# Performance work log

Measured on AMD Instinct MI355X. Metric: run time of the kernel, lower is better.

Reference implementation:

```python
import jax, jax.numpy as jnp
import numpy as np

B, Q, S, T, HID, NH = 4, 64, 64, 128, 768, 12
HD = HID // NH  # 64
SCALE = 1.0 / (HD ** 0.5)
EPS = 1e-12


def setup_inputs() -> dict:
    key = jax.random.key(0)
    ks = jax.random.split(key, 12)
    std = 0.02
    return {
        "ini_q": jax.random.normal(ks[0], (B, Q, HID), jnp.float32),
        "ini_k": jax.random.normal(ks[1], (B, S, T, HID), jnp.float32),
        "mask": jax.random.randint(ks[2], (B, S, T), 0, 2).astype(jnp.float32),
        "Wq": jax.random.normal(ks[3], (HID, HID), jnp.float32) * std,
        "bq": jnp.zeros((HID,), jnp.float32),
        "Wk": jax.random.normal(ks[4], (HID, HID), jnp.float32) * std,
        "bk": jnp.zeros((HID,), jnp.float32),
        "Wv": jax.random.normal(ks[5], (HID, HID), jnp.float32) * std,
        "bv": jnp.zeros((HID,), jnp.float32),
        "Wo": jax.random.normal(ks[6], (HID, HID), jnp.float32) * std,
        "bo": jnp.zeros((HID,), jnp.float32),
        "gamma": jnp.ones((HID,), jnp.float32),
        "beta": jnp.zeros((HID,), jnp.float32),
    }


def reference(ini_q, ini_k, mask, Wq, bq, Wk, bk, Wv, bv, Wo, bo, gamma, beta):
    b, q_num, _ = ini_q.shape
    _, s_num, t_num, _ = ini_k.shape
    # projections (torch Linear: x @ W.T + b; here W stored pre-transposed)
    q = (ini_q @ Wq + bq).reshape(b, q_num, NH, HD)          # [b,q,h,d]
    k = (ini_k @ Wk + bk).reshape(b, s_num, t_num, NH, HD)   # [b,s,t,h,d]
    v = (ini_k @ Wv + bv).reshape(b, s_num, t_num, NH, HD)
    # non-aligned path: scores [b,h,q,s,t]
    scores = jnp.einsum('bqhd,bsthd->bhqst', q, k) * SCALE
    scores = scores + mask[:, None, None, :, :] * (-10000.0)
    alpha = jax.nn.softmax(scores, axis=-1)
    res = jnp.einsum('bhqst,bsthd->bqshd', alpha, v)          # [b,q,s,h,d]
    res = res.reshape(b, q_num, s_num, NH * HD)
    res = res @ Wo + bo                                        # [b,q,s,hid]
    # LayerNorm over last dim
    mu = jnp.mean(res, axis=-1, keepdims=True)
    var = jnp.var(res, axis=-1, keepdims=True)
    return (res - mu) / jnp.sqrt(var + EPS) * gamma + beta
```

## Files before the change

### kernel.cpp

```cpp
#include <hip/hip_runtime.h>
#include <cstdint>
#include <cstddef>
#include <type_traits>

#define HID 768
#define NB 4
#define NQ 64
#define NS 64
#define NT 128
#define NHEAD 12
#define HD 64

typedef __attribute__((ext_vector_type(8))) short bf16x8;
typedef __attribute__((ext_vector_type(4))) float f32x4;

__device__ __forceinline__ unsigned short f2bf(float f) {
    union { float f; uint32_t u; } c; c.f = f;
    uint32_t x = c.u;
    uint32_t r = (x + 0x7FFFu + ((x >> 16) & 1u)) >> 16;
    return (unsigned short)r;
}

__device__ __forceinline__ f32x4 mfma16(bf16x8 a, bf16x8 b, f32x4 c) {
    return __builtin_amdgcn_mfma_f32_16x16x32_bf16(a, b, c, 0, 0, 0);
}

__device__ __forceinline__ void gload_lds16(const void* g, void* l) {
    __builtin_amdgcn_global_load_lds(
        (const __attribute__((address_space(1))) unsigned int*)g,
        (__attribute__((address_space(3))) unsigned int*)l, 16, 0, 0);
}

__global__ __launch_bounds__(256) void cast4_f32_bf16(const float* __restrict__ in,
                                                      unsigned short* __restrict__ out, int n4) {
    int i = blockIdx.x * 256 + threadIdx.x;
    if (i < n4) {
        float4 v = ((const float4*)in)[i];
        ushort4 o;
        o.x = f2bf(v.x); o.y = f2bf(v.y); o.z = f2bf(v.z); o.w = f2bf(v.w);
        ((ushort4*)out)[i] = o;
    }
}

__global__ __launch_bounds__(256) void transpose_cast_768(const float* __restrict__ W,
                                                          unsigned short* __restrict__ Wt) {
    __shared__ float t[32][33];
    int bx = blockIdx.x % 24, by = blockIdx.x / 24;
    int n0 = bx * 32, k0 = by * 32;
    int tx = threadIdx.x & 31, ty = threadIdx.x >> 5;
#pragma unroll
    for (int i = 0; i < 4; ++i)
        t[ty + i * 8][tx] = W[(size_t)(k0 + ty + i * 8) * 768 + n0 + tx];
    __syncthreads();
#pragma unroll
    for (int i = 0; i < 4; ++i)
        Wt[(size_t)(n0 + ty + i * 8) * 768 + k0 + tx] = f2bf(t[tx][ty + i * 8]);
}

template <typename CT>
__global__ __launch_bounds__(256) void gemm_bt_768(const unsigned short* __restrict__ A,
                                                   const unsigned short* __restrict__ Bt,
                                                   const float* __restrict__ bias,
                                                   CT* __restrict__ C, int M) {
    constexpr int K = 768, N = 768;
    __shared__ __align__(16) unsigned short As[128 * 32];
    __shared__ __align__(16) unsigned short Bs[128 * 32];

    int tid = threadIdx.x;
    int w = tid >> 6, l = tid & 63;
    int li = l & 15, g = l >> 4;
    int wm = w >> 1, wn = w & 1;
    int nb = blockIdx.x % (N / 128);
    int mb = blockIdx.x / (N / 128);

    const unsigned short* Ab = A + (size_t)mb * 128 * K;
    const unsigned short* Bb = Bt + (size_t)nb * 128 * K;

    int ch0 = w * 128 + l, ch1 = w * 128 + 64 + l;
    int r0 = ch0 >> 2, c0 = ch0 & 3;
    int r1 = ch1 >> 2, c1 = ch1 & 3;
    char* lA0 = (char*)As + w * 2048;
    char* lA1 = (char*)As + w * 2048 + 1024;
    char* lB0 = (char*)Bs + w * 2048;
    char* lB1 = (char*)Bs + w * 2048 + 1024;

    f32x4 acc[4][4];
#pragma unroll
    for (int mi = 0; mi < 4; ++mi)
#pragma unroll
        for (int ni = 0; ni < 4; ++ni) acc[mi][ni] = (f32x4){0.f, 0.f, 0.f, 0.f};

    for (int kt = 0; kt < K / 32; ++kt) {
        int k0 = kt * 32;
        __syncthreads();
        gload_lds16(Ab + (size_t)r0 * K + k0 + c0 * 8, lA0);
        gload_lds16(Ab + (size_t)r1 * K + k0 + c1 * 8, lA1);
        gload_lds16(Bb + (size_t)r0 * K + k0 + c0 * 8, lB0);
        gload_lds16(Bb + (size_t)r1 * K + k0 + c1 * 8, lB1);
        __syncthreads();

        bf16x8 af[4], bb[4];
#pragma unroll
        for (int mi = 0; mi < 4; ++mi)
            af[mi] = *(const bf16x8*)&As[(wm * 64 + mi * 16 + li) * 32 + g * 8];
#pragma unroll
        for (int ni = 0; ni < 4; ++ni)
            bb[ni] = *(const bf16x8*)&Bs[(wn * 64 + ni * 16 + li) * 32 + g * 8];
#pragma unroll
        for (int mi = 0; mi < 4; ++mi)
#pragma unroll
            for (int ni = 0; ni < 4; ++ni)
                acc[mi][ni] = mfma16(af[mi], bb[ni], acc[mi][ni]);
    }

    int rowb = mb * 128 + wm * 64;
    int colb = nb * 128 + wn * 64;
#pragma unroll
    for (int ni = 0; ni < 4; ++ni) {
        float bv = bias[colb + ni * 16 + li];
        int col = colb + ni * 16 + li;
#pragma unroll
        for (int mi = 0; mi < 4; ++mi) {
#pragma unroll
            for (int r = 0; r < 4; ++r) {
                int row = rowb + mi * 16 + g * 4 + r;
                float v = acc[mi][ni][r] + bv;
                if constexpr (std::is_same_v<CT, unsigned short>)
                    C[(size_t)row * N + col] = f2bf(v);
                else
                    C[(size_t)row * N + col] = v;
            }
        }
    }
}

__global__ __launch_bounds__(256) void attn_bsh(const unsigned short* __restrict__ Qp,
                                                const unsigned short* __restrict__ Kb,
                                                const unsigned short* __restrict__ Vb,
                                                const float* __restrict__ mask,
                                                unsigned short* __restrict__ res) {
    __shared__ __align__(16) unsigned short Kl[128 * 72];
    __shared__ __align__(16) unsigned short VT[64 * 136];
    __shared__ __align__(16) unsigned short QA[64 * 136];

    int bid = blockIdx.x;
    int h = bid % NHEAD;
    int bs = bid / NHEAD;
    int s = bs % NS;
    int b = bs / NS;

    int tid = threadIdx.x, w = tid >> 6, l = tid & 63;
    int li = l & 15, g = l >> 4;

    const unsigned short* Qg = Qp + (size_t)(b * NQ) * HID + h * HD;
#pragma unroll
    for (int it = 0; it < 2; ++it) {
        int idx = it * 256 + tid;
        int q = idx >> 3, c = idx & 7;
        *(uint4*)&QA[q * 72 + c * 8] = *(const uint4*)&Qg[(size_t)q * HID + c * 8];
    }
    const unsigned short* Kg = Kb + ((size_t)(b * NS + s) * NT) * HID + h * HD;
#pragma unroll
    for (int it = 0; it < 4; ++it) {
        int idx = it * 256 + tid;
        int t = idx >> 3, c = idx & 7;
        *(uint4*)&Kl[t * 72 + c * 8] = *(const uint4*)&Kg[(size_t)t * HID + c * 8];
    }
    const unsigned short* Vg = Vb + ((size_t)(b * NS + s) * NT) * HID + h * HD;
#pragma unroll
    for (int it = 0; it < 4; ++it) {
        int idx = it * 256 + tid;
        int t = idx >> 3, c = idx & 7;
        uint4 raw = *(const uint4*)&Vg[(size_t)t * HID + c * 8];
        const unsigned short* e = (const unsigned short*)&raw;
#pragma unroll
        for (int j = 0; j < 8; ++j) VT[(c * 8 + j) * 136 + t] = e[j];
    }
    __syncthreads();

    bf16x8 aq0 = *(const bf16x8*)&QA[(w * 16 + li) * 72 + g * 8];
    bf16x8 aq1 = *(const bf16x8*)&QA[(w * 16 + li) * 72 + 32 + g * 8];
    f32x4 sc[8];
#pragma unroll
    for (int tc = 0; tc < 8; ++tc) {
        sc[tc] = (f32x4){0.f, 0.f, 0.f, 0.f};
        bf16x8 b0 = *(const bf16x8*)&Kl[(tc * 16 + li) * 72 + g * 8];
        sc[tc] = mfma16(aq0, b0, sc[tc]);
        bf16x8 b1 = *(const bf16x8*)&Kl[(tc * 16 + li) * 72 + 32 + g * 8];
        sc[tc] = mfma16(aq1, b1, sc[tc]);
    }

    const float* mrow = mask + (size_t)(b * NS + s) * NT;
    float mv[8];
#pragma unroll
    for (int tc = 0; tc < 8; ++tc) mv[tc] = mrow[tc * 16 + li] * -10000.0f;

    float p[8][4];
    float rmax[4] = {-3.0e38f, -3.0e38f, -3.0e38f, -3.0e38f};
#pragma unroll
    for (int tc = 0; tc < 8; ++tc)
#pragma unroll
        for (int r = 0; r < 4; ++r) {
            float v = sc[tc][r] * 0.125f + mv[tc];
            p[tc][r] = v;
            rmax[r] = fmaxf(rmax[r], v);
        }
#pragma unroll
    for (int r = 0; r < 4; ++r)
#pragma unroll
        for (int m = 1; m < 16; m <<= 1)
            rmax[r] = fmaxf(rmax[r], __shfl_xor(rmax[r], m, 64));

    float rsum[4] = {0.f, 0.f, 0.f, 0.f};
#pragma unroll
    for (int tc = 0; tc < 8; ++tc)
#pragma unroll
        for (int r = 0; r < 4; ++r) {
            float e = __expf(p[tc][r] - rmax[r]);
            p[tc][r] = e;
            rsum[r] += e;
        }
#pragma unroll
    for (int r = 0; r < 4; ++r)
#pragma unroll
        for (int m = 1; m < 16; m <<= 1)
            rsum[r] += __shfl_xor(rsum[r], m, 64);
    float rinv[4];
#pragma unroll
    for (int r = 0; r < 4; ++r) rinv[r] = 1.0f / rsum[r];

    __syncthreads();
#pragma unroll
    for (int tc = 0; tc < 8; ++tc)
#pragma unroll
        for (int r = 0; r < 4; ++r)
            QA[(w * 16 + g * 4 + r) * 136 + tc * 16 + li] = f2bf(p[tc][r] * rinv[r]);
    __syncthreads();

    bf16x8 pa[4];
#pragma unroll
    for (int ks = 0; ks < 4; ++ks)
        pa[ks] = *(const bf16x8*)&QA[(w * 16 + li) * 136 + ks * 32 + g * 8];
    f32x4 o[4];
#pragma unroll
    for (int dc = 0; dc < 4; ++dc) {
        o[dc] = (f32x4){0.f, 0.f, 0.f, 0.f};
#pragma unroll
        for (int ks = 0; ks < 4; ++ks) {
            bf16x8 bv = *(const bf16x8*)&VT[(dc * 16 + li) * 136 + ks * 32 + g * 8];
            o[dc] = mfma16(pa[ks], bv, o[dc]);
        }
    }

#pragma unroll
    for (int dc = 0; dc < 4; ++dc) {
#pragma unroll
        for (int r = 0; r < 4; ++r) {
            int q = w * 16 + g * 4 + r;
            int d = dc * 16 + li;
            res[((size_t)(b * NQ + q) * NS + s) * HID + h * HD + d] = f2bf(o[dc][r]);
        }
    }
}

__global__ __launch_bounds__(256) void ln_768(const float* __restrict__ X,
                                              const float* __restrict__ gamma,
                                              const float* __restrict__ beta,
                                              float* __restrict__ out) {
    int w = threadIdx.x >> 6, l = threadIdx.x & 63;
    size_t row = (size_t)blockIdx.x * 4 + w;
    const float4* xr = (const float4*)(X + row * 768);
    float4 v[3];
    float s = 0.f, sq = 0.f;
#pragma unroll
    for (int j = 0; j < 3; ++j) {
        v[j] = xr[l + j * 64];
        s += v[j].x + v[j].y + v[j].z + v[j].w;
        sq += v[j].x * v[j].x + v[j].y * v[j].y + v[j].z * v[j].z + v[j].w * v[j].w;
    }
#pragma unroll
    for (int m = 32; m >= 1; m >>= 1) {
        s += __shfl_xor(s, m, 64);
        sq += __shfl_xor(sq, m, 64);
    }
    float mu = s * (1.0f / 768.0f);
    float var = sq * (1.0f / 768.0f) - mu * mu;
    float rstd = rsqrtf(fmaxf(var, 0.0f) + 1e-12f);
    const float4* g4 = (const float4*)gamma;
    const float4* b4 = (const float4*)beta;
    float4* o4 = (float4*)(out + row * 768);
#pragma unroll
    for (int j = 0; j < 3; ++j) {
        float4 gg = g4[l + j * 64], bb = b4[l + j * 64];
        float4 r;
        r.x = (v[j].x - mu) * rstd * gg.x + bb.x;
        r.y = (v[j].y - mu) * rstd * gg.y + bb.y;
        r.z = (v[j].z - mu) * rstd * gg.z + bb.z;
        r.w = (v[j].w - mu) * rstd * gg.w + bb.w;
        o4[l + j * 64] = r;
    }
}

extern "C" void kernel_launch(void* const* d_in, const int* in_sizes, int n_in,
                              void* d_out, int out_size, void* d_ws, size_t ws_size,
                              hipStream_t stream) {
    const float* ini_q = (const float*)d_in[0];
    const float* ini_k = (const float*)d_in[1];
    const float* mask  = (const float*)d_in[2];
    const float* Wq = (const float*)d_in[3];
    const float* bq = (const float*)d_in[4];
    const float* Wk = (const float*)d_in[5];
    const float* bk = (const float*)d_in[6];
    const float* Wv = (const float*)d_in[7];
    const float* bv = (const float*)d_in[8];
    const float* Wo = (const float*)d_in[9];
    const float* bo = (const float*)d_in[10];
    const float* gamma = (const float*)d_in[11];
    const float* beta  = (const float*)d_in[12];
    float* out = (float*)d_out;

    constexpr size_t SZ_X = (size_t)32768 * 768 * 2;
    constexpr size_t SZ_R = (size_t)16384 * 768 * 2;
    constexpr size_t SZ_Q = (size_t)256 * 768 * 2;
    constexpr size_t SZ_W = (size_t)768 * 768 * 2;

    char* base = (char*)d_ws;
    unsigned short* X   = (unsigned short*)(base);
    unsigned short* Kb  = (unsigned short*)(base + SZ_X);
    unsigned short* Vb  = (unsigned short*)(base + 2 * SZ_X);
    unsigned short* res = (unsigned short*)(base + 3 * SZ_X);
    unsigned short* Xq  = (unsigned short*)(base + 3 * SZ_X + SZ_R);
    unsigned short* Qp  = (unsigned short*)(base + 3 * SZ_X + SZ_R + SZ_Q);
    unsigned short* WqT = (unsigned short*)(base + 3 * SZ_X + SZ_R + 2 * SZ_Q);
    unsigned short* WkT = (unsigned short*)((char*)WqT + SZ_W);
    unsigned short* WvT = (unsigned short*)((char*)WqT + 2 * SZ_W);
    unsigned short* WoT = (unsigned short*)((char*)WqT + 3 * SZ_W);
    float* res2 = (float*)(base);

    cast4_f32_bf16<<<24576, 256, 0, stream>>>(ini_k, X, 6291456);
    cast4_f32_bf16<<<192, 256, 0, stream>>>(ini_q, Xq, 49152);
    transpose_cast_768<<<576, 256, 0, stream>>>(Wq, WqT);
    transpose_cast_768<<<576, 256, 0, stream>>>(Wk, WkT);
    transpose_cast_768<<<576, 256, 0, stream>>>(Wv, WvT);
    transpose_cast_768<<<576, 256, 0, stream>>>(Wo, WoT);

    gemm_bt_768<unsigned short><<<dim3(2 * 6), 256, 0, stream>>>(Xq, WqT, bq, Qp, 256);
    gemm_bt_768<unsigned short><<<dim3(256 * 6), 256, 0, stream>>>(X, WkT, bk, Kb, 32768);
    gemm_bt_768<unsigned short><<<dim3(256 * 6), 256, 0, stream>>>(X, WvT, bv, Vb, 32768);

    attn_bsh<<<dim3(NB * NS * NHEAD), 256, 0, stream>>>(Qp, Kb, Vb, mask, res);

    gemm_bt_768<float><<<dim3(128 * 6), 256, 0, stream>>>(res, WoT, bo, res2, 16384);
    ln_768<<<dim3(4096), 256, 0, stream>>>(res2, gamma, beta, out);
}
```

Before: 421.2 us.

## Double-buffer GEMM LDS tiles, fuse K/V projections, and swizzle block order

The bf16 GEMM kernel now double-buffers its LDS tiles, so the global-to-LDS load for the next k-step is issued before the MFMA work on the current one, which hides load latency and removes one barrier per iteration. The K and V projections are merged into one GEMM over a concatenated 1536-wide transposed weight, and the epilogue routes each column to the K or V output, so the input X is streamed once instead of twice. Block IDs are remapped in groups of 8 when the grid size allows, presumably for better cache or XCD locality. LDS use per block doubles, which may reduce occupancy.

```diff
diff --git a/kernel.cpp b/kernel.cpp
--- a/kernel.cpp
+++ b/kernel.cpp
@@ -57,32 +57,50 @@
         Wt[(size_t)(n0 + ty + i * 8) * 768 + k0 + tx] = f2bf(t[tx][ty + i * 8]);
 }
 
-template <typename CT>
-__global__ __launch_bounds__(256) void gemm_bt_768(const unsigned short* __restrict__ A,
+template <typename CT, bool SPLIT>
+__global__ __launch_bounds__(256) void gemm_bt_2ph(const unsigned short* __restrict__ A,
                                                    const unsigned short* __restrict__ Bt,
-                                                   const float* __restrict__ bias,
-                                                   CT* __restrict__ C, int M) {
-    constexpr int K = 768, N = 768;
-    __shared__ __align__(16) unsigned short As[128 * 32];
-    __shared__ __align__(16) unsigned short Bs[128 * 32];
+                                                   const float* __restrict__ bias0,
+                                                   const float* __restrict__ bias1,
+                                                   CT* __restrict__ C0,
+                                                   CT* __restrict__ C1,
+                                                   int ncb) {
+    constexpr int K = 768;
+    constexpr int NKT = K / 32;
+    __shared__ __align__(16) unsigned short As[2][128 * 32];
+    __shared__ __align__(16) unsigned short Bs[2][128 * 32];
 
     int tid = threadIdx.x;
     int w = tid >> 6, l = tid & 63;
     int li = l & 15, g = l >> 4;
     int wm = w >> 1, wn = w & 1;
-    int nb = blockIdx.x % (N / 128);
-    int mb = blockIdx.x / (N / 128);
+
+    int nwg = gridDim.x, bid = blockIdx.x;
+    if ((nwg & 7) == 0) {
+        int cpx = nwg >> 3;
+        bid = (bid & 7) * cpx + (bid >> 3);
+    }
+    int nb = bid % ncb, mb = bid / ncb;
 
     const unsigned short* Ab = A + (size_t)mb * 128 * K;
     const unsigned short* Bb = Bt + (size_t)nb * 128 * K;
 
-    int ch0 = w * 128 + l, ch1 = w * 128 + 64 + l;
+    int ch0 = w * 128 + l, ch1 = ch0 + 64;
     int r0 = ch0 >> 2, c0 = ch0 & 3;
     int r1 = ch1 >> 2, c1 = ch1 & 3;
-    char* lA0 = (char*)As + w * 2048;
-    char* lA1 = (char*)As + w * 2048 + 1024;
-    char* lB0 = (char*)Bs + w * 2048;
-    char* lB1 = (char*)Bs + w * 2048 + 1024;
+
+#define STAGE(bufi, kt)                                                              \
+    do {                                                                             \
+        int k0_ = (kt) * 32;                                                         \
+        gload_lds16(Ab + (size_t)r0 * K + k0_ + c0 * 8,                              \
+                    (char*)(&As[bufi][0]) + w * 2048);                               \
+        gload_lds16(Ab + (size_t)r1 * K + k0_ + c1 * 8,                              \
+                    (char*)(&As[bufi][0]) + w * 2048 + 1024);                        \
+        gload_lds16(Bb + (size_t)r0 * K + k0_ + c0 * 8,                              \
+                    (char*)(&Bs[bufi][0]) + w * 2048);                               \
+        gload_lds16(Bb + (size_t)r1 * K + k0_ + c1 * 8,                              \
+                    (char*)(&Bs[bufi][0]) + w * 2048 + 1024);                        \
+    } while (0)
 
     f32x4 acc[4][4];
 #pragma unroll
@@ -90,35 +108,48 @@
 #pragma unroll
         for (int ni = 0; ni < 4; ++ni) acc[mi][ni] = (f32x4){0.f, 0.f, 0.f, 0.f};
 
-    for (int kt = 0; kt < K / 32; ++kt) {
-        int k0 = kt * 32;
+#define COMPUTE(bufi)                                                                \
+    do {                                                                             \
+        bf16x8 af[4], bb[4];                                                         \
+        _Pragma("unroll") for (int mi = 0; mi < 4; ++mi)                             \
+            af[mi] = *(const bf16x8*)&As[bufi][(wm * 64 + mi * 16 + li) * 32 + g * 8];\
+        _Pragma("unroll") for (int ni = 0; ni < 4; ++ni)                             \
+            bb[ni] = *(const bf16x8*)&Bs[bufi][(wn * 64 + ni * 16 + li) * 32 + g * 8];\
+        _Pragma("unroll") for (int mi = 0; mi < 4; ++mi)                             \
+            _Pragma("unroll") for (int ni = 0; ni < 4; ++ni)                         \
+                acc[mi][ni] = mfma16(af[mi], bb[ni], acc[mi][ni]);                   \
+    } while (0)
+
+    STAGE(0, 0);
+    __syncthreads();
+    for (int kt = 0; kt < NKT - 2; kt += 2) {
+        STAGE(1, kt + 1);
+        COMPUTE(0);
         __syncthreads();
-        gload_lds16(Ab + (size_t)r0 * K + k0 + c0 * 8, lA0);
-        gload_lds16(Ab + (size_t)r1 * K + k0 + c1 * 8, lA1);
-        gload_lds16(Bb + (size_t)r0 * K + k0 + c0 * 8, lB0);
-        gload_lds16(Bb + (size_t)r1 * K + k0 + c1 * 8, lB1);
+        STAGE(0, kt + 2);
+        COMPUTE(1);
         __syncthreads();
-
-        bf16x8 af[4], bb[4];
-#pragma unroll
-        for (int mi = 0; mi < 4; ++mi)
-            af[mi] = *(const bf16x8*)&As[(wm * 64 + mi * 16 + li) * 32 + g * 8];
-#pragma unroll
-        for (int ni = 0; ni < 4; ++ni)
-            bb[ni] = *(const bf16x8*)&Bs[(wn * 64 + ni * 16 + li) * 32 + g * 8];
-#pragma unroll
-        for (int mi = 0; mi < 4; ++mi)
-#pragma unroll
-            for (int ni = 0; ni < 4; ++ni)
-                acc[mi][ni] = mfma16(af[mi], bb[ni], acc[mi][ni]);
-    }
+    }
+    STAGE(1, NKT - 1);
+    COMPUTE(0);
+    __syncthreads();
+    COMPUTE(1);
+#undef STAGE
+#undef COMPUTE
 
     int rowb = mb * 128 + wm * 64;
     int colb = nb * 128 + wn * 64;
 #pragma unroll
     for (int ni = 0; ni < 4; ++ni) {
-        float bv = bias[colb + ni * 16 + li];
         int col = colb + ni * 16 + li;
+        CT* Cp;
+        float bv;
+        int ccol;
+        if (SPLIT && col >= 768) {
+            Cp = C1; bv = bias1[col - 768]; ccol = col - 768;
+        } else {
+            Cp = C0; bv = bias0[col]; ccol = col;
+        }
 #pragma unroll
         for (int mi = 0; mi < 4; ++mi) {
 #pragma unroll
@@ -126,9 +157,9 @@
                 int row = rowb + mi * 16 + g * 4 + r;
                 float v = acc[mi][ni][r] + bv;
                 if constexpr (std::is_same_v<CT, unsigned short>)
-                    C[(size_t)row * N + col] = f2bf(v);
+                    Cp[(size_t)row * 768 + ccol] = f2bf(v);
                 else
-                    C[(size_t)row * N + col] = v;
+                    Cp[(size_t)row * 768 + ccol] = v;
             }
         }
     }
@@ -332,24 +363,25 @@
     unsigned short* Xq  = (unsigned short*)(base + 3 * SZ_X + SZ_R);
     unsigned short* Qp  = (unsigned short*)(base + 3 * SZ_X + SZ_R + SZ_Q);
     unsigned short* WqT = (unsigned short*)(base + 3 * SZ_X + SZ_R + 2 * SZ_Q);
-    unsigned short* WkT = (unsigned short*)((char*)WqT + SZ_W);
-    unsigned short* WvT = (unsigned short*)((char*)WqT + 2 * SZ_W);
+    unsigned short* KVt = (unsigned short*)((char*)WqT + SZ_W);
     unsigned short* WoT = (unsigned short*)((char*)WqT + 3 * SZ_W);
     float* res2 = (float*)(base);
 
     cast4_f32_bf16<<<24576, 256, 0, stream>>>(ini_k, X, 6291456);
     cast4_f32_bf16<<<192, 256, 0, stream>>>(ini_q, Xq, 49152);
     transpose_cast_768<<<576, 256, 0, stream>>>(Wq, WqT);
-    transpose_cast_768<<<576, 256, 0, stream>>>(Wk, WkT);
-    transpose_cast_768<<<576, 256, 0, stream>>>(Wv, WvT);
+    transpose_cast_768<<<576, 256, 0, stream>>>(Wk, KVt);
+    transpose_cast_768<<<576, 256, 0, stream>>>(Wv, KVt + 768 * 768);
     transpose_cast_768<<<576, 256, 0, stream>>>(Wo, WoT);
 
-    gemm_bt_768<unsigned short><<<dim3(2 * 6), 256, 0, stream>>>(Xq, WqT, bq, Qp, 256);
-    gemm_bt_768<unsigned short><<<dim3(256 * 6), 256, 0, stream>>>(X, WkT, bk, Kb, 32768);
-    gemm_bt_768<unsigned short><<<dim3(256 * 6), 256, 0, stream>>>(X, WvT, bv, Vb, 32768);
+    gemm_bt_2ph<unsigned short, false><<<dim3(2 * 6), 256, 0, stream>>>(
+        Xq, WqT, bq, nullptr, Qp, nullptr, 6);
+    gemm_bt_2ph<unsigned short, true><<<dim3(256 * 12), 256, 0, stream>>>(
+        X, KVt, bk, bv, Kb, Vb, 12);
 
     attn_bsh<<<dim3(NB * NS * NHEAD), 256, 0, stream>>>(Qp, Kb, Vb, mask, res);
 
-    gemm_bt_768<float><<<dim3(128 * 6), 256, 0, stream>>>(res, WoT, bo, res2, 16384);
+    gemm_bt_2ph<float, false><<<dim3(128 * 6), 256, 0, stream>>>(
+        res, WoT, bo, nullptr, res2, nullptr, 6);
     ln_768<<<dim3(4096), 256, 0, stream>>>(res2, gamma, beta, out);
 }
```

Result: no change. 425.1 us (+0.9%).
